# Performance work log

Hardware: AMD Instinct MI355X
Metric: run time of the kernel (lower is better)

## Reference

```python
import jax, jax.numpy as jnp
import numpy as np

V, E, H, L, S, T = 100000, 256, 512, 50000, 512, 64


def setup_inputs() -> dict:
    key = jax.random.key(0)
    ks = jax.random.split(key, 14)
    s = 0.02
    return {
        "encoder_outputs": jax.random.normal(ks[0], (1, S, H), jnp.float32),
        "enc_h0": jax.random.normal(ks[1], (1, 1, H), jnp.float32),
        "enc_c0": jax.random.normal(ks[2], (1, 1, H), jnp.float32),
        "emb_table": jax.random.normal(ks[3], (V, E), jnp.float32) * s,
        "W_attn": jax.random.normal(ks[4], (H, E), jnp.float32) * s,
        "b_attn": jnp.zeros((H,), jnp.float32),
        "W_ih": jax.random.normal(ks[5], (4 * H, H), jnp.float32) * s,
        "W_hh": jax.random.normal(ks[6], (4 * H, H), jnp.float32) * s,
        "b_ih": jnp.zeros((4 * H,), jnp.float32),
        "b_hh": jnp.zeros((4 * H,), jnp.float32),
        "W_out": jax.random.normal(ks[7], (L, H), jnp.float32) * s,
        "b_out": jnp.zeros((L,), jnp.float32),
        "word_inputs": jax.random.randint(ks[8], (T,), 0, V),
        "labels": jax.random.randint(ks[9], (T,), 0, L),
    }


def reference(encoder_outputs, enc_h0, enc_c0, emb_table, W_attn, b_attn,
              W_ih, W_hh, b_ih, b_hh, W_out, b_out, word_inputs, labels):
    # batch == 1 throughout (matches forward_train); dropout is identity (eval).
    enc = encoder_outputs[0]          # [S, H]
    h0 = enc_h0[0, 0]                 # [H]  (bidirect hidden already flattened to 1x1xH)
    c0 = enc_c0[0, 0]                 # [H]

    def step(carry, xs):
        h, c = carry
        widx, label = xs
        e = emb_table[widx]                               # [E]   embedding lookup
        q = W_attn @ e + b_attn                           # [H]   attn projection (Linear)
        alphas = jax.nn.softmax(enc @ q)                  # [S]   bmm + softmax
        ctx = alphas @ enc                                # [H]   bmm -> context
        # single-step LSTM (PyTorch gate order: i, f, g, o)
        gates = W_ih @ ctx + b_ih + W_hh @ h + b_hh       # [4H]
        i, f, g, o = jnp.split(gates, 4)
        i = jax.nn.sigmoid(i); f = jax.nn.sigmoid(f)
        g = jnp.tanh(g);       o = jax.nn.sigmoid(o)
        c2 = f * c + i * g
        h2 = o * jnp.tanh(c2)
        logits = W_out @ h2 + b_out                       # [L]   hidden2tag
        ls = jax.nn.log_softmax(logits)
        # NLLLoss(ignore_index=0, reduction='sum')
        step_loss = jnp.where(label == 0, jnp.float32(0.0), -ls[label])
        return (h2, c2), step_loss

    (_, _), losses = jax.lax.scan(step, (h0, c0),
                                  (word_inputs, labels))
    return jnp.sum(losses)
```

## Files before the change

### kernel.cpp

```cpp
#include <hip/hip_runtime.h>
#include <hip/hip_bf16.h>

#define V_ 100000
#define E_ 256
#define H_ 512
#define L_ 50000
#define S_ 512
#define T_ 64
#define NB_ 782
#define NBP_ 784
#define NWG_ 32
#define NPF_ 128

typedef short bf16x8 __attribute__((ext_vector_type(8)));
typedef float f32x4 __attribute__((ext_vector_type(4)));

__device__ __forceinline__ float sigm(float x){ return 1.0f/(1.0f+__expf(-x)); }
__device__ __forceinline__ float tanh_fast(float x){
    x = fminf(fmaxf(x, -15.f), 15.f);
    float e = __expf(2.f * x);
    return __fdividef(e - 1.f, e + 1.f);
}
__device__ __forceinline__ unsigned bf16rne(float x){
    unsigned u = __float_as_uint(x);
    return (u + 0x7fffu + ((u >> 16) & 1u)) >> 16;
}
__device__ __forceinline__ float bcast(float v, int l){
    return __uint_as_float(__builtin_amdgcn_readlane(__float_as_uint(v), l));
}

__global__ __launch_bounds__(256) void k_attn(
    const float* __restrict__ enc, const float* __restrict__ emb,
    const float* __restrict__ W_attn, const float* __restrict__ b_attn,
    const int* __restrict__ word_inputs, float* __restrict__ ctx_out)
{
    __shared__ float e_l[E_];
    __shared__ float q_l[H_];
    __shared__ float sc[S_];
    __shared__ float red[8];
    const int t = blockIdx.x, tid = threadIdx.x;
    const int widx = word_inputs[t];

    e_l[tid] = emb[(long)widx * E_ + tid];
    __syncthreads();

    for (int rr = 0; rr < 2; ++rr) {
        int r = tid + rr * 256;
        const float4* wrow = (const float4*)(W_attn + r * E_);
        const float4* ev = (const float4*)e_l;
        float acc = b_attn[r];
        #pragma unroll 8
        for (int j = 0; j < E_ / 4; ++j) {
            float4 w = wrow[j], e4 = ev[j];
            acc += w.x*e4.x + w.y*e4.y + w.z*e4.z + w.w*e4.w;
        }
        q_l[r] = acc;
    }
    __syncthreads();

    for (int rr = 0; rr < 2; ++rr) {
        int s = tid + rr * 256;
        const float4* er = (const float4*)(enc + s * H_);
        const float4* qv = (const float4*)q_l;
        float acc = 0.f;
        #pragma unroll 8
        for (int j = 0; j < H_ / 4; ++j) {
            float4 a = er[j], b = qv[j];
            acc += a.x*b.x + a.y*b.y + a.z*b.z + a.w*b.w;
        }
        sc[s] = acc;
    }
    __syncthreads();

    float m = fmaxf(sc[tid], sc[tid + 256]);
    for (int off = 32; off; off >>= 1) m = fmaxf(m, __shfl_down(m, off));
    if ((tid & 63) == 0) red[tid >> 6] = m;
    __syncthreads();
    if (tid == 0) red[4] = fmaxf(fmaxf(red[0], red[1]), fmaxf(red[2], red[3]));
    __syncthreads();
    m = red[4];
    float e0 = __expf(sc[tid] - m), e1 = __expf(sc[tid + 256] - m);
    sc[tid] = e0; sc[tid + 256] = e1;
    float ssum = e0 + e1;
    for (int off = 32; off; off >>= 1) ssum += __shfl_down(ssum, off);
    if ((tid & 63) == 0) red[tid >> 6] = ssum;
    __syncthreads();
    if (tid == 0) red[5] = red[0] + red[1] + red[2] + red[3];
    __syncthreads();
    float inv = 1.0f / red[5];

    for (int rr = 0; rr < 2; ++rr) {
        int h = tid + rr * 256;
        float acc = 0.f;
        #pragma unroll 4
        for (int s = 0; s < S_; ++s) acc += sc[s] * enc[s * H_ + h];
        ctx_out[t * H_ + h] = acc * inv;
    }
}

__global__ __launch_bounds__(256) void k_gatepre(
    const float* __restrict__ ctx, const float* __restrict__ W_ih,
    const float* __restrict__ b_ih, const float* __restrict__ b_hh,
    float* __restrict__ A_pre)
{
    __shared__ float ctx_t[H_ * 65];
    __shared__ float w_l[8 * H_];
    const int tid = threadIdx.x;
    const int r0 = blockIdx.x * 8;

    for (int i = 0; i < 32; ++i) {
        int p = tid + i * 256;
        int t = p >> 7, k4 = p & 127;
        float4 v = ((const float4*)ctx)[p];
        ctx_t[(k4*4+0)*65 + t] = v.x;
        ctx_t[(k4*4+1)*65 + t] = v.y;
        ctx_t[(k4*4+2)*65 + t] = v.z;
        ctx_t[(k4*4+3)*65 + t] = v.w;
    }
    for (int i = 0; i < 4; ++i) {
        int p = tid + i * 256;
        int row = p >> 7, k4 = p & 127;
        float4 v = ((const float4*)W_ih)[(r0 + row) * (H_/4) + k4];
        float* dst = &w_l[row * H_ + k4 * 4];
        dst[0]=v.x; dst[1]=v.y; dst[2]=v.z; dst[3]=v.w;
    }
    __syncthreads();

    const int t = tid & 63, half = tid >> 6;
    const float* w0 = &w_l[(half*2+0) * H_];
    const float* w1 = &w_l[(half*2+1) * H_];
    float acc0 = 0.f, acc1 = 0.f;
    #pragma unroll 4
    for (int k = 0; k < H_; ++k) {
        float cv = ctx_t[k * 65 + t];
        acc0 += w0[k] * cv;
        acc1 += w1[k] * cv;
    }
    int ra = r0 + half * 2, rb = ra + 1;
    A_pre[t * 2048 + ra] = acc0 + b_ih[ra] + b_hh[ra];
    A_pre[t * 2048 + rb] = acc1 + b_ih[rb] + b_hh[rb];
}

__global__ __launch_bounds__(512, 2) void k_lstm(
    const float* __restrict__ W_hh, const float* __restrict__ A_pre,
    const float* __restrict__ h0, const float* __restrict__ c0,
    float* __restrict__ h_buf, const float* __restrict__ W_out)
{
    const int tid = threadIdx.x, wg = blockIdx.x;

    if (wg >= NWG_) {
        const long total = (long)L_ * H_ / 4;
        const long stride = (long)NPF_ * 512;
        const float4* src = (const float4*)W_out;
        float acc = 0.f;
        for (long i = (long)(wg - NWG_) * 512 + tid; i < total; i += stride) {
            float4 v = src[i];
            acc += v.x + v.y + v.z + v.w;
        }
        asm volatile("" :: "v"(acc));
        return;
    }

    __shared__ float A_l[T_ * 64];
    __shared__ float red[2][8][64];

    const int base = wg * 16;
    const int lane = tid & 63;
    const int ks   = tid >> 6;
    const int G = ((lane >> 4) << 9) + base + (lane & 15);

    float w[64];
    {
        const float4* wsrc = (const float4*)(W_hh + (long)G * H_ + ks * 64);
        #pragma unroll
        for (int i = 0; i < 16; ++i) {
            float4 v = wsrc[i];
            w[4*i+0]=v.x; w[4*i+1]=v.y; w[4*i+2]=v.z; w[4*i+3]=v.w;
        }
    }
    #pragma unroll
    for (int i = 0; i < 64; ++i) asm volatile("" : "+v"(w[i]));

    for (int i = 0; i < 8; ++i) {
        int p = tid + i * 512;
        int tt = p >> 6, rr = p & 63;
        A_l[p] = A_pre[tt * 2048 + ((rr >> 4) << 9) + base + (rr & 15)];
    }
    float c_reg = 0.f;
    if (tid < 16) c_reg = c0[base + tid];
    __syncthreads();

    const unsigned SENT = 0xFFFFFFFFu;

    for (int t = 0; t < T_; ++t) {
        float hv;
        if (t == 0) {
            hv = h0[ks * 64 + lane];
        } else {
            const unsigned* hb = (const unsigned*)h_buf + (t - 1) * H_ + ks * 64;
            unsigned u = __hip_atomic_load(hb + lane, __ATOMIC_RELAXED,
                                           __HIP_MEMORY_SCOPE_AGENT);
            while (u == SENT) {
                __builtin_amdgcn_s_sleep(1);
                u = __hip_atomic_load(hb + lane, __ATOMIC_RELAXED,
                                      __HIP_MEMORY_SCOPE_AGENT);
            }
            hv = __uint_as_float(u);
        }

        float a0 = 0.f, a1 = 0.f, a2 = 0.f, a3 = 0.f;
        #pragma unroll
        for (int j = 0; j < 64; j += 4) {
            a0 += bcast(hv, j+0) * w[j+0];
            a1 += bcast(hv, j+1) * w[j+1];
            a2 += bcast(hv, j+2) * w[j+2];
            a3 += bcast(hv, j+3) * w[j+3];
        }
        red[t & 1][ks][lane] = (a0 + a1) + (a2 + a3);
        __syncthreads();

        if (ks == 0) {
            float s = A_l[t * 64 + lane];
            #pragma unroll
            for (int k2 = 0; k2 < 8; ++k2) s += red[t & 1][k2][lane];
            float gf_ = __shfl_down(s, 16);
            float gg_ = __shfl_down(s, 32);
            float go_ = __shfl_down(s, 48);
            if (lane < 16) {
                float gi = sigm(s);
                float gf = sigm(gf_);
                float gg = tanh_fast(gg_);
                float go = sigm(go_);
                float c2 = gf * c_reg + gi * gg;
                c_reg = c2;
                float h2 = go * tanh_fast(c2);
                __hip_atomic_store((unsigned*)h_buf + t * H_ + base + lane,
                                   __float_as_uint(h2),
                                   __ATOMIC_RELAXED, __HIP_MEMORY_SCOPE_AGENT);
            }
        }
    }
}

__global__ __launch_bounds__(256) void k_out(
    const float* __restrict__ W_out, const float* __restrict__ b_out,
    const float* __restrict__ h_buf, const int* __restrict__ labels,
    float* __restrict__ pm, float* __restrict__ ps, float* __restrict__ ll)
{
    __shared__ __align__(16) unsigned char smem[65536];
    const int tid = threadIdx.x;
    const int r0 = blockIdx.x * 64;
    const int lane = tid & 63, w = tid >> 6;
    const int g = lane >> 4, li = lane & 15;

    for (int i = 0; i < 32; ++i) {
        int p = tid + i * 256;
        int t = p >> 7, k4 = p & 127;
        float4 v = ((const float4*)h_buf)[p];
        unsigned p01 = bf16rne(v.x) | (bf16rne(v.y) << 16);
        unsigned p23 = bf16rne(v.z) | (bf16rne(v.w) << 16);
        unsigned byte = (unsigned)(t * 1024 + k4 * 8) ^ ((unsigned)(t & 7) << 4);
        *(uint2*)(smem + byte) = make_uint2(p01, p23);
    }

    f32x4 acc0 = {0.f,0.f,0.f,0.f}, acc1 = {0.f,0.f,0.f,0.f};
    f32x4 acc2 = {0.f,0.f,0.f,0.f}, acc3 = {0.f,0.f,0.f,0.f};
    __syncthreads();

    int rrow = r0 + w * 16 + li;
    int rw = rrow < L_ ? rrow : (L_ - 1);
    const float* ap = W_out + (long)rw * H_ + g * 8;

    #pragma unroll
    for (int kk = 0; kk < 16; ++kk) {
        float4 va = *(const float4*)(ap + kk * 32);
        float4 vb = *(const float4*)(ap + kk * 32 + 4);
        union { unsigned u[4]; bf16x8 v; } A;
        A.u[0] = bf16rne(va.x) | (bf16rne(va.y) << 16);
        A.u[1] = bf16rne(va.z) | (bf16rne(va.w) << 16);
        A.u[2] = bf16rne(vb.x) | (bf16rne(vb.y) << 16);
        A.u[3] = bf16rne(vb.z) | (bf16rne(vb.w) << 16);

        #pragma unroll
        for (int nt = 0; nt < 4; ++nt) {
            int t = nt * 16 + li;
            unsigned byte = (unsigned)(t * 1024 + kk * 64 + g * 16)
                          ^ ((unsigned)(t & 7) << 4);
            bf16x8 B = *(const bf16x8*)(smem + byte);
            f32x4* accp = (nt == 0) ? &acc0 : (nt == 1) ? &acc1
                        : (nt == 2) ? &acc2 : &acc3;
            *accp = __builtin_amdgcn_mfma_f32_16x16x32_bf16(A.v, B, *accp, 0, 0, 0);
        }
    }
    __syncthreads();

    float* lg   = (float*)smem;
    float* redb = (float*)(smem + 64 * 65 * 4);
    float* gmax = redb + 256;

    #pragma unroll
    for (int nt = 0; nt < 4; ++nt) {
        const f32x4 a = (nt == 0) ? acc0 : (nt == 1) ? acc1
                      : (nt == 2) ? acc2 : acc3;
        int t = nt * 16 + li;
        #pragma unroll
        for (int q = 0; q < 4; ++q) {
            int rloc = w * 16 + g * 4 + q;
            int r = r0 + rloc;
            float v = -1e30f;
            if (r < L_) v = a[q] + b_out[r];
            lg[rloc * 65 + t] = v;
        }
    }
    __syncthreads();

    const int t = tid & 63, part = tid >> 6;
    float m = -1e30f;
    #pragma unroll
    for (int r16 = 0; r16 < 16; ++r16)
        m = fmaxf(m, lg[(part*16 + r16)*65 + t]);
    redb[part*64 + t] = m;
    __syncthreads();
    if (part == 0)
        gmax[t] = fmaxf(fmaxf(redb[t], redb[64+t]), fmaxf(redb[128+t], redb[192+t]));
    __syncthreads();
    float gm = gmax[t];
    float s = 0.f;
    #pragma unroll
    for (int r16 = 0; r16 < 16; ++r16)
        s += __expf(lg[(part*16 + r16)*65 + t] - gm);
    __syncthreads();
    redb[part*64 + t] = s;
    __syncthreads();
    if (part == 0) {
        pm[t * NBP_ + blockIdx.x] = gm;
        ps[t * NBP_ + blockIdx.x] = redb[t] + redb[64+t] + redb[128+t] + redb[192+t];
        int lb = labels[t];
        if (lb >= r0 && lb < r0 + 64) ll[t] = lg[(lb - r0)*65 + t];
    }
}

__global__ __launch_bounds__(256) void k_final(
    const float* __restrict__ pm, const float* __restrict__ ps,
    const float* __restrict__ ll, const int* __restrict__ labels,
    float* __restrict__ out)
{
    __shared__ float rbuf[8];
    const int t = blockIdx.x, tid = threadIdx.x;
    float m = -1e30f;
    for (int b = tid; b < NB_; b += 256) m = fmaxf(m, pm[t * NBP_ + b]);
    for (int off = 32; off; off >>= 1) m = fmaxf(m, __shfl_down(m, off));
    if ((tid & 63) == 0) rbuf[tid >> 6] = m;
    __syncthreads();
    if (tid == 0) rbuf[4] = fmaxf(fmaxf(rbuf[0], rbuf[1]), fmaxf(rbuf[2], rbuf[3]));
    __syncthreads();
    float M = rbuf[4];
    __syncthreads();
    float s = 0.f;
    for (int b = tid; b < NB_; b += 256)
        s += ps[t * NBP_ + b] * __expf(pm[t * NBP_ + b] - M);
    for (int off = 32; off; off >>= 1) s += __shfl_down(s, off);
    if ((tid & 63) == 0) rbuf[tid >> 6] = s;
    __syncthreads();
    if (tid == 0) {
        float S = rbuf[0] + rbuf[1] + rbuf[2] + rbuf[3];
        int lb = labels[t];
        if (lb != 0) {
            float loss = -(ll[t] - M - __logf(S));
            atomicAdd(out, loss);
        }
    }
}

extern "C" void kernel_launch(void* const* d_in, const int* in_sizes, int n_in,
                              void* d_out, int out_size, void* d_ws, size_t ws_size,
                              hipStream_t stream)
{
    (void)in_sizes; (void)n_in; (void)out_size; (void)ws_size;
    const float* enc    = (const float*)d_in[0];
    const float* h0     = (const float*)d_in[1];
    const float* c0     = (const float*)d_in[2];
    const float* emb    = (const float*)d_in[3];
    const float* W_attn = (const float*)d_in[4];
    const float* b_attn = (const float*)d_in[5];
    const float* W_ih   = (const float*)d_in[6];
    const float* W_hh   = (const float*)d_in[7];
    const float* b_ih   = (const float*)d_in[8];
    const float* b_hh   = (const float*)d_in[9];
    const float* W_out  = (const float*)d_in[10];
    const float* b_out  = (const float*)d_in[11];
    const int* widx     = (const int*)d_in[12];
    const int* labels   = (const int*)d_in[13];
    float* out = (float*)d_out;

    char* ws = (char*)d_ws;
    float* ctx   = (float*)(ws + 0);
    float* A_pre = (float*)(ws + 131072);
    float* h_buf = (float*)(ws + 655360);
    float* pm    = (float*)(ws + 786688);
    float* ps    = (float*)(ws + 987392);
    float* ll    = (float*)(ws + 1188096);

    hipMemsetAsync(h_buf, 0xFF, T_ * H_ * sizeof(float), stream);
    hipMemsetAsync(out, 0, sizeof(float), stream);

    k_attn<<<T_, 256, 0, stream>>>(enc, emb, W_attn, b_attn, widx, ctx);
    k_gatepre<<<256, 256, 0, stream>>>(ctx, W_ih, b_ih, b_hh, A_pre);
    k_lstm<<<NWG_ + NPF_, 512, 0, stream>>>(W_hh, A_pre, h0, c0, h_buf, W_out);
    k_out<<<NB_, 256, 0, stream>>>(W_out, b_out, h_buf, labels, pm, ps, ll);
    k_final<<<T_, 256, 0, stream>>>(pm, ps, ll, labels, out);
}
```

Before: 237.1 us.

## Restructure LSTM recurrence so each wave owns rows and reduces via shuffles

The recurrent W_hh matvec is reorganised so that each wave holds the full 512-wide slice of 8 gate rows (two hidden units) in registers. Each wave does its own butterfly shuffle reduction, which removes the per-step workgroup barrier and the LDS cross-wave reduction. The hidden state is read with 64-bit atomic loads and a sentinel check, and the polling drops the sleep. This shortens the serial per-step critical path, at the cost of more shuffle instructions and tighter register pressure (launch bound changed to 1 block per SIMD set).

```diff
diff --git a/kernel.cpp b/kernel.cpp
--- a/kernel.cpp
+++ b/kernel.cpp
@@ -25,9 +25,6 @@
     unsigned u = __float_as_uint(x);
     return (u + 0x7fffu + ((u >> 16) & 1u)) >> 16;
 }
-__device__ __forceinline__ float bcast(float v, int l){
-    return __uint_as_float(__builtin_amdgcn_readlane(__float_as_uint(v), l));
-}
 
 __global__ __launch_bounds__(256) void k_attn(
     const float* __restrict__ enc, const float* __restrict__ emb,
@@ -141,7 +138,18 @@
     A_pre[t * 2048 + rb] = acc1 + b_ih[rb] + b_hh[rb];
 }
 
-__global__ __launch_bounds__(512, 2) void k_lstm(
+#define LD64(p) __hip_atomic_load((p), __ATOMIC_RELAXED, __HIP_MEMORY_SCOPE_AGENT)
+#define BAD(x) ((((unsigned)(x)) == 0xFFFFFFFFu) | (((unsigned)((x) >> 32)) == 0xFFFFFFFFu))
+#define LOADW(r) \
+    float4 Wa##r, Wb##r; \
+    { const float* wp_ = W_hh + (long)((((r) >> 1) * 512) + rowbase + ((r) & 1)) * H_ + lane * 8; \
+      Wa##r = *(const float4*)wp_; Wb##r = *(const float4*)(wp_ + 4); } \
+    asm volatile("" : "+v"(Wa##r.x), "+v"(Wa##r.y), "+v"(Wa##r.z), "+v"(Wa##r.w), \
+                      "+v"(Wb##r.x), "+v"(Wb##r.y), "+v"(Wb##r.z), "+v"(Wb##r.w));
+#define DOT(r) float s##r = Wa##r.x*hv0 + Wa##r.y*hv1 + Wa##r.z*hv2 + Wa##r.w*hv3 \
+                          + Wb##r.x*hv4 + Wb##r.y*hv5 + Wb##r.z*hv6 + Wb##r.w*hv7;
+
+__global__ __launch_bounds__(512, 1) void k_lstm(
     const float* __restrict__ W_hh, const float* __restrict__ A_pre,
     const float* __restrict__ h0, const float* __restrict__ c0,
     float* __restrict__ h_buf, const float* __restrict__ W_out)
@@ -161,83 +169,72 @@
         return;
     }
 
-    __shared__ float A_l[T_ * 64];
-    __shared__ float red[2][8][64];
-
-    const int base = wg * 16;
+    __shared__ float A_l[T_ * 8 * 8];
+
     const int lane = tid & 63;
-    const int ks   = tid >> 6;
-    const int G = ((lane >> 4) << 9) + base + (lane & 15);
-
-    float w[64];
-    {
-        const float4* wsrc = (const float4*)(W_hh + (long)G * H_ + ks * 64);
-        #pragma unroll
-        for (int i = 0; i < 16; ++i) {
-            float4 v = wsrc[i];
-            w[4*i+0]=v.x; w[4*i+1]=v.y; w[4*i+2]=v.z; w[4*i+3]=v.w;
-        }
-    }
-    #pragma unroll
-    for (int i = 0; i < 64; ++i) asm volatile("" : "+v"(w[i]));
+    const int wv   = tid >> 6;
+    const int rowbase = wg * 16 + wv * 2;
+
+    LOADW(0) LOADW(1) LOADW(2) LOADW(3)
+    LOADW(4) LOADW(5) LOADW(6) LOADW(7)
 
     for (int i = 0; i < 8; ++i) {
         int p = tid + i * 512;
-        int tt = p >> 6, rr = p & 63;
-        A_l[p] = A_pre[tt * 2048 + ((rr >> 4) << 9) + base + (rr & 15)];
+        int g = p & 3, u = (p >> 2) & 1, wvv = (p >> 3) & 7, tt = p >> 6;
+        A_l[p] = A_pre[tt * 2048 + g * 512 + wg * 16 + wvv * 2 + u];
     }
     float c_reg = 0.f;
-    if (tid < 16) c_reg = c0[base + tid];
-    __syncthreads();
-
-    const unsigned SENT = 0xFFFFFFFFu;
+    if (lane < 2) c_reg = c0[rowbase + lane];
+    __syncthreads();
 
     for (int t = 0; t < T_; ++t) {
-        float hv;
+        float4 Av = make_float4(0.f, 0.f, 0.f, 0.f);
+        if (lane < 2) Av = *(const float4*)&A_l[((t * 8 + wv) << 3) + (lane << 2)];
+
+        float hv0, hv1, hv2, hv3, hv4, hv5, hv6, hv7;
         if (t == 0) {
-            hv = h0[ks * 64 + lane];
+            const float4* hp = (const float4*)h0 + lane * 2;
+            float4 ha = hp[0], hbv = hp[1];
+            hv0=ha.x; hv1=ha.y; hv2=ha.z; hv3=ha.w;
+            hv4=hbv.x; hv5=hbv.y; hv6=hbv.z; hv7=hbv.w;
         } else {
-            const unsigned* hb = (const unsigned*)h_buf + (t - 1) * H_ + ks * 64;
-            unsigned u = __hip_atomic_load(hb + lane, __ATOMIC_RELAXED,
-                                           __HIP_MEMORY_SCOPE_AGENT);
-            while (u == SENT) {
-                __builtin_amdgcn_s_sleep(1);
-                u = __hip_atomic_load(hb + lane, __ATOMIC_RELAXED,
-                                      __HIP_MEMORY_SCOPE_AGENT);
+            const unsigned long long* hb =
+                (const unsigned long long*)(h_buf + (t - 1) * H_) + lane * 4;
+            unsigned long long pa = LD64(hb + 0), pb = LD64(hb + 1);
+            unsigned long long pc = LD64(hb + 2), pd = LD64(hb + 3);
+            while (BAD(pa) | BAD(pb) | BAD(pc) | BAD(pd)) {
+                if (BAD(pa)) pa = LD64(hb + 0);
+                if (BAD(pb)) pb = LD64(hb + 1);
+                if (BAD(pc)) pc = LD64(hb + 2);
+                if (BAD(pd)) pd = LD64(hb + 3);
             }
-            hv = __uint_as_float(u);
-        }
-
-        float a0 = 0.f, a1 = 0.f, a2 = 0.f, a3 = 0.f;
+            hv0 = __uint_as_float((unsigned)pa); hv1 = __uint_as_float((unsigned)(pa >> 32));
+            hv2 = __uint_as_float((unsigned)pb); hv3 = __uint_as_float((unsigned)(pb >> 32));
+            hv4 = __uint_as_float((unsigned)pc); hv5 = __uint_as_float((unsigned)(pc >> 32));
+            hv6 = __uint_as_float((unsigned)pd); hv7 = __uint_as_float((unsigned)(pd >> 32));
+        }
+
+        DOT(0) DOT(1) DOT(2) DOT(3) DOT(4) DOT(5) DOT(6) DOT(7)
+
         #pragma unroll
-        for (int j = 0; j < 64; j += 4) {
-            a0 += bcast(hv, j+0) * w[j+0];
-            a1 += bcast(hv, j+1) * w[j+1];
-            a2 += bcast(hv, j+2) * w[j+2];
-            a3 += bcast(hv, j+3) * w[j+3];
-        }
-        red[t & 1][ks][lane] = (a0 + a1) + (a2 + a3);
-        __syncthreads();
-
-        if (ks == 0) {
-            float s = A_l[t * 64 + lane];
-            #pragma unroll
-            for (int k2 = 0; k2 < 8; ++k2) s += red[t & 1][k2][lane];
-            float gf_ = __shfl_down(s, 16);
-            float gg_ = __shfl_down(s, 32);
-            float go_ = __shfl_down(s, 48);
-            if (lane < 16) {
-                float gi = sigm(s);
-                float gf = sigm(gf_);
-                float gg = tanh_fast(gg_);
-                float go = sigm(go_);
-                float c2 = gf * c_reg + gi * gg;
-                c_reg = c2;
-                float h2 = go * tanh_fast(c2);
-                __hip_atomic_store((unsigned*)h_buf + t * H_ + base + lane,
-                                   __float_as_uint(h2),
-                                   __ATOMIC_RELAXED, __HIP_MEMORY_SCOPE_AGENT);
-            }
+        for (int off = 1; off < 64; off <<= 1) {
+            s0 += __shfl_xor(s0, off); s1 += __shfl_xor(s1, off);
+            s2 += __shfl_xor(s2, off); s3 += __shfl_xor(s3, off);
+            s4 += __shfl_xor(s4, off); s5 += __shfl_xor(s5, off);
+            s6 += __shfl_xor(s6, off); s7 += __shfl_xor(s7, off);
+        }
+
+        if (lane < 2) {
+            float ri = ((lane == 0) ? s0 : s1) + Av.x;
+            float rf = ((lane == 0) ? s2 : s3) + Av.y;
+            float rg = ((lane == 0) ? s4 : s5) + Av.z;
+            float ro = ((lane == 0) ? s6 : s7) + Av.w;
+            float c2 = sigm(rf) * c_reg + sigm(ri) * tanh_fast(rg);
+            c_reg = c2;
+            float h2 = sigm(ro) * tanh_fast(c2);
+            __hip_atomic_store((unsigned*)h_buf + t * H_ + rowbase + lane,
+                               __float_as_uint(h2),
+                               __ATOMIC_RELAXED, __HIP_MEMORY_SCOPE_AGENT);
         }
     }
 }
```

Result: slower. 550.7 us (+132.2%).
